# Performance work log

Measured on AMD Instinct MI355X. Metric: run time of the kernel, lower is better.

The kernel has to match this reference:

```python
import jax, jax.numpy as jnp
import numpy as np


def setup_inputs() -> dict:
    key = jax.random.key(0)
    ks = jax.random.split(key, 8)
    B, H, W, D, U = 128, 16, 48, 512, 512
    s = 1.0 / np.sqrt(D)
    return {
        "dec_hidden": jax.random.normal(ks[0], (B, D), jnp.float32),
        "enc_output": jax.random.normal(ks[1], (B, H, W, D), jnp.float32),
        "W1_w": jax.random.normal(ks[2], (D, U), jnp.float32) * s,
        "W1_b": jnp.zeros((U,), jnp.float32),
        "W2_w": jax.random.normal(ks[3], (D, U), jnp.float32) * s,
        "W2_b": jnp.zeros((U,), jnp.float32),
        "V_w": jax.random.normal(ks[4], (U, 1), jnp.float32) * (1.0 / np.sqrt(U)),
        "V_b": jnp.zeros((1,), jnp.float32),
    }


def reference(dec_hidden, enc_output, W1_w, W1_b, W2_w, W2_b, V_w, V_b):
    # dec_hidden: [B, Dd] -> [B, 1, 1, Dd]
    dec = dec_hidden[:, None, None, :]
    # W1(enc_output): [B, H, W, U]; W2(dec): [B, 1, 1, U] (broadcast add)
    h = jnp.tanh(jnp.einsum('bhwd,du->bhwu', enc_output, W1_w) + W1_b
                 + (dec @ W2_w + W2_b))
    # V(.) -> score [B, H, W, 1]
    score = jnp.einsum('bhwu,uo->bhwo', h, V_w) + V_b
    # softmax over axis=1 (H axis), matching tf.keras softmax(score, axis=1)
    attention_weights = jax.nn.softmax(score, axis=1)
    # context: sum over spatial axes -> [B, D]
    context_vector = jnp.sum(attention_weights * enc_output, axis=(1, 2))
    return context_vector, attention_weights
```

## Files before the change

kernel.cpp:

```cpp
#include <hip/hip_runtime.h>
#include <hip/hip_bf16.h>

typedef __attribute__((ext_vector_type(8))) short short8;
typedef __attribute__((ext_vector_type(4))) float f32x4;
typedef unsigned short ushort;

#define BB 128
#define HHH 16
#define WWW 48
#define DD 512
#define UU 512
#define ROWS_PER_B (HHH * WWW)
#define MTOT (BB * ROWS_PER_B)
#define BM 64
#define BN 256
#define BK 64

__device__ __forceinline__ ushort f2bf(float f) {
    return (ushort)((__float_as_uint(f) + 0x8000u) >> 16);
}

__device__ __forceinline__ void gload_lds16(const ushort* g, ushort* l) {
    __builtin_amdgcn_global_load_lds(
        (const __attribute__((address_space(1))) unsigned int*)(const void*)g,
        (__attribute__((address_space(3))) unsigned int*)(void*)l,
        16, 0, 0);
}

__global__ __launch_bounds__(256) void prep_kernel(
        const float* __restrict__ w1, const float* __restrict__ dec,
        const float* __restrict__ w2, const float* __restrict__ w1b,
        const float* __restrict__ w2b,
        ushort* __restrict__ w1p, float* __restrict__ dproj) {
    const int t = threadIdx.x;
    if (blockIdx.x < 64) {
        __shared__ __align__(16) ushort tile[64 * 72];
        const int u0 = (blockIdx.x & 7) * 64;
        const int kc = blockIdx.x >> 3;
        const int ul = t & 63;
        const int db = t >> 6;
#pragma unroll
        for (int i = 0; i < 16; ++i) {
            const int d = db + i * 4;
            tile[ul * 72 + d] = f2bf(w1[(size_t)(kc * 64 + d) * UU + u0 + ul]);
        }
        __syncthreads();
        const int u = t >> 2;
        const int s = (t & 3) * 2;
        const int x = u & 7;
        short8 v0 = *(const short8*)&tile[u * 72 + s * 8];
        short8 v1 = *(const short8*)&tile[u * 72 + s * 8 + 8];
        *(short8*)&w1p[(size_t)kc * 32768 + (u0 + u) * 64 + (( s      ^ x)) * 8] = v0;
        *(short8*)&w1p[(size_t)kc * 32768 + (u0 + u) * 64 + (((s + 1) ^ x)) * 8] = v1;
    } else {
        const int g = blockIdx.x - 64;
        const int b = g >> 1;
        const int u = (g & 1) * 256 + t;
        float acc = 0.f;
#pragma unroll 8
        for (int d = 0; d < DD; ++d)
            acc += dec[b * DD + d] * w2[(size_t)d * UU + u];
        dproj[b * UU + u] = acc + w1b[u] + w2b[u];
    }
}

__global__ __launch_bounds__(256, 4) void score_kernel(
        const float* __restrict__ enc, const ushort* __restrict__ w1p,
        const float* __restrict__ dproj, const float* __restrict__ vw,
        float* __restrict__ scorep) {
    __shared__ __align__(16) ushort Bb[BN * BK];
    __shared__ __align__(16) ushort Ab[BM * BK];

    const int tid  = threadIdx.x;
    const int lane = tid & 63;
    const int wave = tid >> 6;
    const int mbase = blockIdx.x * BM;
    const int half  = blockIdx.y;
    const int b = mbase / ROWS_PER_B;

    const int lrow = lane & 15;
    const int kgrp = lane >> 4;

    const int ar  = tid >> 2;
    const int ac  = (tid & 3) * 2;
    const float* abase = enc + (size_t)(mbase + ar) * DD + ac * 8;
    const int s0p = ( ac      ^ (ar & 7)) * 8;
    const int s1p = ((ac + 1) ^ (ar & 7)) * 8;
    const ushort* bsrc0 = w1p + half * 16384 + tid * 8;

    f32x4 acc[4][4] = {};

    for (int kc = 0; kc < 8; ++kc) {
        const ushort* bsrc = bsrc0 + (size_t)kc * 32768;
#pragma unroll
        for (int i = 0; i < 8; ++i)
            gload_lds16(bsrc + i * 2048, &Bb[tid * 8 + i * 2048]);
        {
            const float* asrc = abase + kc * 64;
            float4 a0 = ((const float4*)asrc)[0];
            float4 a1 = ((const float4*)asrc)[1];
            float4 a2 = ((const float4*)asrc)[2];
            float4 a3 = ((const float4*)asrc)[3];
            short8 w0, w1v;
            ushort* p0 = (ushort*)&w0; ushort* p1 = (ushort*)&w1v;
            p0[0]=f2bf(a0.x); p0[1]=f2bf(a0.y); p0[2]=f2bf(a0.z); p0[3]=f2bf(a0.w);
            p0[4]=f2bf(a1.x); p0[5]=f2bf(a1.y); p0[6]=f2bf(a1.z); p0[7]=f2bf(a1.w);
            p1[0]=f2bf(a2.x); p1[1]=f2bf(a2.y); p1[2]=f2bf(a2.z); p1[3]=f2bf(a2.w);
            p1[4]=f2bf(a3.x); p1[5]=f2bf(a3.y); p1[6]=f2bf(a3.z); p1[7]=f2bf(a3.w);
            *(short8*)&Ab[ar * 64 + s0p] = w0;
            *(short8*)&Ab[ar * 64 + s1p] = w1v;
        }
        __syncthreads();

#pragma unroll
        for (int kk = 0; kk < 2; ++kk) {
            const int sub = kk * 4 + kgrp;
            short8 afr[4], bfr[4];
#pragma unroll
            for (int ms = 0; ms < 4; ++ms) {
                const int r = ms * 16 + lrow;
                afr[ms] = *(const short8*)&Ab[r * 64 + (sub ^ (r & 7)) * 8];
            }
#pragma unroll
            for (int uf = 0; uf < 4; ++uf) {
                const int u = wave * 64 + uf * 16 + lrow;
                bfr[uf] = *(const short8*)&Bb[u * 64 + (sub ^ (u & 7)) * 8];
            }
#pragma unroll
            for (int ms = 0; ms < 4; ++ms)
#pragma unroll
                for (int uf = 0; uf < 4; ++uf)
                    acc[ms][uf] = __builtin_amdgcn_mfma_f32_16x16x32_bf16(
                        afr[ms], bfr[uf], acc[ms][uf], 0, 0, 0);
        }
        __syncthreads();
    }

    float part[4][4] = {};
#pragma unroll
    for (int uf = 0; uf < 4; ++uf) {
        const int u = half * 256 + wave * 64 + uf * 16 + lrow;
        const float cadd = dproj[b * UU + u];
        const float vwe  = vw[u];
#pragma unroll
        for (int ms = 0; ms < 4; ++ms)
#pragma unroll
            for (int j = 0; j < 4; ++j) {
                float x = acc[ms][uf][j] + cadd;
                x = fminf(fmaxf(x, -15.f), 15.f);
                float e = __expf(2.f * x);
                part[ms][j] += vwe * ((e - 1.f) / (e + 1.f));
            }
    }
#pragma unroll
    for (int off = 1; off < 16; off <<= 1)
#pragma unroll
        for (int ms = 0; ms < 4; ++ms)
#pragma unroll
            for (int j = 0; j < 4; ++j)
                part[ms][j] += __shfl_xor(part[ms][j], off, 64);

    float* scr = (float*)&Ab[0];
    if (lrow == 0) {
#pragma unroll
        for (int ms = 0; ms < 4; ++ms)
#pragma unroll
            for (int j = 0; j < 4; ++j)
                scr[wave * 64 + ms * 16 + kgrp * 4 + j] = part[ms][j];
    }
    __syncthreads();
    if (tid < 64)
        scorep[(size_t)half * MTOT + mbase + tid] =
            scr[tid] + scr[64 + tid] + scr[128 + tid] + scr[192 + tid];
}

__global__ __launch_bounds__(512) void ctx_kernel(
        const float* __restrict__ scorep, const float* __restrict__ enc,
        const float* __restrict__ vb,
        float* __restrict__ attn, float* __restrict__ partial) {
    __shared__ float sl[ROWS_PER_B];
    __shared__ float al[ROWS_PER_B];
    const int q = blockIdx.x;
    const int b = blockIdx.y;
    const int t = threadIdx.x;

    const float vbv = vb[0];
    for (int i = t; i < ROWS_PER_B; i += 512)
        sl[i] = scorep[b * ROWS_PER_B + i] + scorep[MTOT + b * ROWS_PER_B + i] + vbv;
    __syncthreads();

    if (t < WWW) {
        float v[HHH];
        float m = -1e30f;
#pragma unroll
        for (int h = 0; h < HHH; ++h) { v[h] = sl[h * WWW + t]; m = fmaxf(m, v[h]); }
        float sum = 0.f;
#pragma unroll
        for (int h = 0; h < HHH; ++h) { v[h] = __expf(v[h] - m); sum += v[h]; }
        const float inv = 1.f / sum;
#pragma unroll
        for (int h = 0; h < HHH; ++h) al[h * WWW + t] = v[h] * inv;
    }
    __syncthreads();

    const int rb = q * 192;
    for (int i = t; i < 192; i += 512)
        attn[b * ROWS_PER_B + rb + i] = al[rb + i];

    const int r0 = t >> 7;
    const int d4 = (t & 127) * 4;
    float4 acc = {0.f, 0.f, 0.f, 0.f};
    const float* ebase = enc + ((size_t)b * ROWS_PER_B + rb) * DD + d4;
#pragma unroll 8
    for (int i = 0; i < 48; ++i) {
        const int r = r0 + i * 4;
        const float a = al[rb + r];
        const float4 e = *(const float4*)(ebase + (size_t)r * DD);
        acc.x += a * e.x; acc.y += a * e.y; acc.z += a * e.z; acc.w += a * e.w;
    }
    *(float4*)(partial + ((size_t)((b * 4 + q) * 4 + r0)) * DD + d4) = acc;
}

__global__ void ctx_reduce_kernel(const float* __restrict__ partial,
                                  float* __restrict__ out) {
    const int qd = blockIdx.x * 256 + threadIdx.x;
    const int b = qd >> 7;
    const int d4 = (qd & 127) * 4;
    float4 s = {0.f, 0.f, 0.f, 0.f};
#pragma unroll
    for (int j = 0; j < 16; ++j) {
        const float4 p = *(const float4*)(partial + ((size_t)(b * 16 + j)) * DD + d4);
        s.x += p.x; s.y += p.y; s.z += p.z; s.w += p.w;
    }
    *(float4*)(out + (size_t)b * DD + d4) = s;
}

extern "C" void kernel_launch(void* const* d_in, const int* in_sizes, int n_in,
                              void* d_out, int out_size, void* d_ws, size_t ws_size,
                              hipStream_t stream) {
    const float* dec = (const float*)d_in[0];
    const float* enc = (const float*)d_in[1];
    const float* w1w = (const float*)d_in[2];
    const float* w1b = (const float*)d_in[3];
    const float* w2w = (const float*)d_in[4];
    const float* w2b = (const float*)d_in[5];
    const float* vw  = (const float*)d_in[6];
    const float* vb  = (const float*)d_in[7];

    float* out = (float*)d_out;
    char* ws = (char*)d_ws;
    ushort* w1p    = (ushort*)(ws);
    float* dproj   = (float*)(ws + (512 << 10));
    float* scorep  = (float*)(ws + (768 << 10));
    float* partial = (float*)(ws + (1536 << 10));

    float* ctx  = out;
    float* attn = out + BB * DD;

    prep_kernel<<<320, 256, 0, stream>>>(w1w, dec, w2w, w1b, w2b, w1p, dproj);
    score_kernel<<<dim3(MTOT / BM, 2), 256, 0, stream>>>(enc, w1p, dproj, vw, scorep);
    ctx_kernel<<<dim3(4, BB), 512, 0, stream>>>(scorep, enc, vb, attn, partial);
    ctx_reduce_kernel<<<64, 256, 0, stream>>>(partial, ctx);
}
```

Baseline: 397.6 us.

## Pre-convert encoder output to swizzled bf16 and double-buffer the score GEMM

Adds a prep pass that converts the whole fp32 encoder tensor once into a tiled, swizzled bf16 buffer in workspace. The score kernel then streams both operands straight into double-buffered LDS with async global-to-LDS loads, and the context kernel reads the bf16 copy instead of fp32. This removes the repeated fp32-to-bf16 conversion per N-half and overlaps loads with MFMA work, in exchange for an extra ~100MB write and read. It also computes the decoder projection with split-K atomics, uses an exp2/rcp tanh, and adds a blocked tile order. Context accuracy drops because enc is now bf16, and the new path only runs if the workspace is large enough.

```diff
diff --git a/kernel.cpp b/kernel.cpp
--- a/kernel.cpp
+++ b/kernel.cpp
@@ -19,7 +19,9 @@
 __device__ __forceinline__ ushort f2bf(float f) {
     return (ushort)((__float_as_uint(f) + 0x8000u) >> 16);
 }
-
+__device__ __forceinline__ float bf2f(ushort u) {
+    return __uint_as_float(((unsigned)u) << 16);
+}
 __device__ __forceinline__ void gload_lds16(const ushort* g, ushort* l) {
     __builtin_amdgcn_global_load_lds(
         (const __attribute__((address_space(1))) unsigned int*)(const void*)g,
@@ -27,7 +29,258 @@
         16, 0, 0);
 }
 
-__global__ __launch_bounds__(256) void prep_kernel(
+__global__ __launch_bounds__(256) void prep2_kernel(
+        const float* __restrict__ enc, const float* __restrict__ w1,
+        const float* __restrict__ dec, const float* __restrict__ w2,
+        ushort* __restrict__ encp, ushort* __restrict__ w1p,
+        float* __restrict__ dproj) {
+    __shared__ __align__(16) char smem[32768];
+    const int t = threadIdx.x;
+    const int bid = blockIdx.x;
+
+    if (bid < 64) {
+        const int u0 = (bid & 7) * 64;
+        const int d0 = (bid >> 3) * 64;
+        const int u  = t & 63;
+        const int bq = t >> 6;
+        float w2r[64];
+#pragma unroll
+        for (int dd = 0; dd < 64; ++dd)
+            w2r[dd] = w2[(size_t)(d0 + dd) * UU + u0 + u];
+        float* decs = (float*)smem;
+        for (int i = t; i < 8192; i += 256)
+            decs[i] = dec[(size_t)(i >> 6) * DD + d0 + (i & 63)];
+        __syncthreads();
+        for (int j = 0; j < 32; ++j) {
+            const float* dr = &decs[(bq * 32 + j) * 64];
+            float s = 0.f;
+#pragma unroll
+            for (int dd = 0; dd < 64; ++dd) s = fmaf(dr[dd], w2r[dd], s);
+            atomicAdd(&dproj[(size_t)(bq * 32 + j) * UU + u0 + u], s);
+        }
+    } else if (bid < 128) {
+        const int pb = bid - 64;
+        ushort* tile = (ushort*)smem;
+        const int u0 = (pb & 7) * 64;
+        const int kc = pb >> 3;
+        const int ul = t & 63;
+        const int db = t >> 6;
+#pragma unroll
+        for (int i = 0; i < 16; ++i) {
+            const int d = db + i * 4;
+            tile[ul * 72 + d] = f2bf(w1[(size_t)(kc * 64 + d) * UU + u0 + ul]);
+        }
+        __syncthreads();
+        const int u = t >> 2;
+        const int s = (t & 3) * 2;
+        const int x = u & 7;
+        short8 v0 = *(const short8*)&tile[u * 72 + s * 8];
+        short8 v1 = *(const short8*)&tile[u * 72 + s * 8 + 8];
+        *(short8*)&w1p[(size_t)kc * 32768 + (u0 + u) * 64 + (( s      ^ x)) * 8] = v0;
+        *(short8*)&w1p[(size_t)kc * 32768 + (u0 + u) * 64 + (((s + 1) ^ x)) * 8] = v1;
+    } else {
+        const int mt  = bid - 128;
+        const int row = t >> 2;
+        const int cb  = (t & 3) * 2;
+        const float* src = enc + ((size_t)mt * 64 + row) * DD + cb * 8;
+        ushort* dst = encp + (size_t)mt * 32768 + row * 64;
+        const int s0 = ( cb      ^ (row & 7)) * 8;
+        const int s1 = ((cb + 1) ^ (row & 7)) * 8;
+#pragma unroll
+        for (int kc = 0; kc < 8; ++kc) {
+            const float* s4 = src + kc * 64;
+            float4 a0 = ((const float4*)s4)[0];
+            float4 a1 = ((const float4*)s4)[1];
+            float4 a2 = ((const float4*)s4)[2];
+            float4 a3 = ((const float4*)s4)[3];
+            short8 w0, w1v;
+            ushort* p0 = (ushort*)&w0; ushort* p1 = (ushort*)&w1v;
+            p0[0]=f2bf(a0.x); p0[1]=f2bf(a0.y); p0[2]=f2bf(a0.z); p0[3]=f2bf(a0.w);
+            p0[4]=f2bf(a1.x); p0[5]=f2bf(a1.y); p0[6]=f2bf(a1.z); p0[7]=f2bf(a1.w);
+            p1[0]=f2bf(a2.x); p1[1]=f2bf(a2.y); p1[2]=f2bf(a2.z); p1[3]=f2bf(a2.w);
+            p1[4]=f2bf(a3.x); p1[5]=f2bf(a3.y); p1[6]=f2bf(a3.z); p1[7]=f2bf(a3.w);
+            *(short8*)&dst[kc * 4096 + s0] = w0;
+            *(short8*)&dst[kc * 4096 + s1] = w1v;
+        }
+    }
+}
+
+__global__ __launch_bounds__(256, 2) void score2_kernel(
+        const ushort* __restrict__ encp, const ushort* __restrict__ w1p,
+        const float* __restrict__ dproj, const float* __restrict__ w1b,
+        const float* __restrict__ w2b, const float* __restrict__ vw,
+        float* __restrict__ scorep) {
+    __shared__ __align__(16) ushort Bb[2][BN * BK];
+    __shared__ __align__(16) ushort Ab[2][BM * BK];
+
+    const int tid  = threadIdx.x;
+    const int lane = tid & 63;
+    const int wave = tid >> 6;
+    const int wg   = blockIdx.x;
+    const int mt   = (wg & 7) * 192 + ((wg >> 3) >> 1);
+    const int half = (wg >> 3) & 1;
+    const int mbase = mt * 64;
+    const int b = mt / 12;
+    const int lrow = lane & 15;
+    const int kgrp = lane >> 4;
+
+    const ushort* asrc0 = encp + (size_t)mt * 32768 + tid * 8;
+    const ushort* bsrc0 = w1p + half * 16384 + tid * 8;
+
+    f32x4 acc[4][4] = {};
+
+    gload_lds16(asrc0,        &Ab[0][tid * 8]);
+    gload_lds16(asrc0 + 2048, &Ab[0][tid * 8 + 2048]);
+#pragma unroll
+    for (int i = 0; i < 8; ++i)
+        gload_lds16(bsrc0 + i * 2048, &Bb[0][tid * 8 + i * 2048]);
+    asm volatile("s_waitcnt vmcnt(0)" ::: "memory");
+    __syncthreads();
+
+    for (int kc = 0; kc < 8; ++kc) {
+        const int cur = kc & 1;
+        if (kc < 7) {
+            const ushort* an = asrc0 + (kc + 1) * 4096;
+            const ushort* bn = bsrc0 + (size_t)(kc + 1) * 32768;
+            gload_lds16(an,        &Ab[cur ^ 1][tid * 8]);
+            gload_lds16(an + 2048, &Ab[cur ^ 1][tid * 8 + 2048]);
+#pragma unroll
+            for (int i = 0; i < 8; ++i)
+                gload_lds16(bn + i * 2048, &Bb[cur ^ 1][tid * 8 + i * 2048]);
+        }
+        const ushort* Bc = &Bb[cur][0];
+        const ushort* Ac = &Ab[cur][0];
+#pragma unroll
+        for (int kk = 0; kk < 2; ++kk) {
+            const int sub = kk * 4 + kgrp;
+            short8 afr[4], bfr[4];
+#pragma unroll
+            for (int ms = 0; ms < 4; ++ms) {
+                const int r = ms * 16 + lrow;
+                afr[ms] = *(const short8*)&Ac[r * 64 + (sub ^ (r & 7)) * 8];
+            }
+#pragma unroll
+            for (int uf = 0; uf < 4; ++uf) {
+                const int u = wave * 64 + uf * 16 + lrow;
+                bfr[uf] = *(const short8*)&Bc[u * 64 + (sub ^ (u & 7)) * 8];
+            }
+#pragma unroll
+            for (int ms = 0; ms < 4; ++ms)
+#pragma unroll
+                for (int uf = 0; uf < 4; ++uf)
+                    acc[ms][uf] = __builtin_amdgcn_mfma_f32_16x16x32_bf16(
+                        afr[ms], bfr[uf], acc[ms][uf], 0, 0, 0);
+        }
+        asm volatile("s_waitcnt vmcnt(0)" ::: "memory");
+        __syncthreads();
+    }
+
+    const float C2 = 2.8853900817779268f;
+    float part[4][4] = {};
+#pragma unroll
+    for (int uf = 0; uf < 4; ++uf) {
+        const int u = half * 256 + wave * 64 + uf * 16 + lrow;
+        const float cadd = dproj[b * UU + u] + w1b[u] + w2b[u];
+        const float vwe  = vw[u];
+#pragma unroll
+        for (int ms = 0; ms < 4; ++ms)
+#pragma unroll
+            for (int j = 0; j < 4; ++j) {
+                float x = acc[ms][uf][j] + cadd;
+                float e = __builtin_amdgcn_exp2f(x * C2);
+                float r = __builtin_amdgcn_rcpf(1.f + e);
+                float h = fmaf(-2.f, r, 1.f);
+                part[ms][j] = fmaf(vwe, h, part[ms][j]);
+            }
+    }
+#pragma unroll
+    for (int off = 1; off < 16; off <<= 1)
+#pragma unroll
+        for (int ms = 0; ms < 4; ++ms)
+#pragma unroll
+            for (int j = 0; j < 4; ++j)
+                part[ms][j] += __shfl_xor(part[ms][j], off, 64);
+
+    float* scr = (float*)&Ab[0][0];
+    if (lrow == 0) {
+#pragma unroll
+        for (int ms = 0; ms < 4; ++ms)
+#pragma unroll
+            for (int j = 0; j < 4; ++j)
+                scr[wave * 64 + ms * 16 + kgrp * 4 + j] = part[ms][j];
+    }
+    __syncthreads();
+    if (tid < 64)
+        scorep[(size_t)half * MTOT + mbase + tid] =
+            scr[tid] + scr[64 + tid] + scr[128 + tid] + scr[192 + tid];
+}
+
+__global__ __launch_bounds__(256) void ctx2_kernel(
+        const float* __restrict__ scorep, const ushort* __restrict__ encp,
+        const float* __restrict__ vb, float* __restrict__ attn,
+        float* __restrict__ partial) {
+    __shared__ float sl[ROWS_PER_B];
+    __shared__ float al[ROWS_PER_B];
+    const int q = blockIdx.x;
+    const int b = blockIdx.y;
+    const int t = threadIdx.x;
+    const float vbv = vb[0];
+    for (int i = t; i < ROWS_PER_B; i += 256)
+        sl[i] = scorep[b * ROWS_PER_B + i] + scorep[MTOT + b * ROWS_PER_B + i] + vbv;
+    __syncthreads();
+    if (t < WWW) {
+        float v[HHH];
+        float m = -1e30f;
+#pragma unroll
+        for (int h = 0; h < HHH; ++h) { v[h] = sl[h * WWW + t]; m = fmaxf(m, v[h]); }
+        float sum = 0.f;
+#pragma unroll
+        for (int h = 0; h < HHH; ++h) { v[h] = __expf(v[h] - m); sum += v[h]; }
+        const float inv = 1.f / sum;
+#pragma unroll
+        for (int h = 0; h < HHH; ++h) al[h * WWW + t] = v[h] * inv;
+    }
+    __syncthreads();
+    if (t < 96) attn[b * ROWS_PER_B + q * 96 + t] = al[q * 96 + t];
+
+    const int rp = t >> 6;
+    const int g8 = t & 63;
+    const int kc = g8 >> 3;
+    float fa[8] = {};
+#pragma unroll 4
+    for (int i = 0; i < 24; ++i) {
+        const int r = q * 96 + rp + i * 4;
+        const float a = al[r];
+        const size_t gr = (size_t)b * ROWS_PER_B + r;
+        const ushort* p = encp + (gr >> 6) * 32768 + kc * 4096 + (gr & 63) * 64
+                        + (((g8 & 7) ^ (r & 7)) * 8);
+        short8 v = *(const short8*)p;
+#pragma unroll
+        for (int j = 0; j < 8; ++j)
+            fa[j] = fmaf(a, bf2f((ushort)v[j]), fa[j]);
+    }
+    float* dst = partial + ((size_t)((b * 8 + q) * 4 + rp)) * DD + g8 * 8;
+    float4 o0 = {fa[0], fa[1], fa[2], fa[3]};
+    float4 o1 = {fa[4], fa[5], fa[6], fa[7]};
+    ((float4*)dst)[0] = o0;
+    ((float4*)dst)[1] = o1;
+}
+
+__global__ void reduce2_kernel(const float* __restrict__ partial,
+                               float* __restrict__ out) {
+    const int qd = blockIdx.x * 256 + threadIdx.x;
+    const int b = qd >> 7;
+    const int d4 = (qd & 127) * 4;
+    float4 s = {0.f, 0.f, 0.f, 0.f};
+#pragma unroll
+    for (int j = 0; j < 32; ++j) {
+        const float4 p = *(const float4*)(partial + ((size_t)(b * 32 + j)) * DD + d4);
+        s.x += p.x; s.y += p.y; s.z += p.z; s.w += p.w;
+    }
+    *(float4*)(out + (size_t)b * DD + d4) = s;
+}
+
+__global__ __launch_bounds__(256) void prep_fb(
         const float* __restrict__ w1, const float* __restrict__ dec,
         const float* __restrict__ w2, const float* __restrict__ w1b,
         const float* __restrict__ w2b,
@@ -64,32 +317,27 @@
     }
 }
 
-__global__ __launch_bounds__(256, 4) void score_kernel(
+__global__ __launch_bounds__(256, 4) void score_fb(
         const float* __restrict__ enc, const ushort* __restrict__ w1p,
         const float* __restrict__ dproj, const float* __restrict__ vw,
         float* __restrict__ scorep) {
     __shared__ __align__(16) ushort Bb[BN * BK];
     __shared__ __align__(16) ushort Ab[BM * BK];
-
     const int tid  = threadIdx.x;
     const int lane = tid & 63;
     const int wave = tid >> 6;
     const int mbase = blockIdx.x * BM;
     const int half  = blockIdx.y;
     const int b = mbase / ROWS_PER_B;
-
     const int lrow = lane & 15;
     const int kgrp = lane >> 4;
-
     const int ar  = tid >> 2;
     const int ac  = (tid & 3) * 2;
     const float* abase = enc + (size_t)(mbase + ar) * DD + ac * 8;
     const int s0p = ( ac      ^ (ar & 7)) * 8;
     const int s1p = ((ac + 1) ^ (ar & 7)) * 8;
     const ushort* bsrc0 = w1p + half * 16384 + tid * 8;
-
     f32x4 acc[4][4] = {};
-
     for (int kc = 0; kc < 8; ++kc) {
         const ushort* bsrc = bsrc0 + (size_t)kc * 32768;
 #pragma unroll
@@ -111,7 +359,6 @@
             *(short8*)&Ab[ar * 64 + s1p] = w1v;
         }
         __syncthreads();
-
 #pragma unroll
         for (int kk = 0; kk < 2; ++kk) {
             const int sub = kk * 4 + kgrp;
@@ -135,7 +382,6 @@
         }
         __syncthreads();
     }
-
     float part[4][4] = {};
 #pragma unroll
     for (int uf = 0; uf < 4; ++uf) {
@@ -159,7 +405,6 @@
 #pragma unroll
             for (int j = 0; j < 4; ++j)
                 part[ms][j] += __shfl_xor(part[ms][j], off, 64);
-
     float* scr = (float*)&Ab[0];
     if (lrow == 0) {
 #pragma unroll
@@ -174,7 +419,7 @@
             scr[tid] + scr[64 + tid] + scr[128 + tid] + scr[192 + tid];
 }
 
-__global__ __launch_bounds__(512) void ctx_kernel(
+__global__ __launch_bounds__(512) void ctx_fb(
         const float* __restrict__ scorep, const float* __restrict__ enc,
         const float* __restrict__ vb,
         float* __restrict__ attn, float* __restrict__ partial) {
@@ -183,12 +428,10 @@
     const int q = blockIdx.x;
     const int b = blockIdx.y;
     const int t = threadIdx.x;
-
     const float vbv = vb[0];
     for (int i = t; i < ROWS_PER_B; i += 512)
         sl[i] = scorep[b * ROWS_PER_B + i] + scorep[MTOT + b * ROWS_PER_B + i] + vbv;
     __syncthreads();
-
     if (t < WWW) {
         float v[HHH];
         float m = -1e30f;
@@ -202,11 +445,9 @@
         for (int h = 0; h < HHH; ++h) al[h * WWW + t] = v[h] * inv;
     }
     __syncthreads();
-
     const int rb = q * 192;
     for (int i = t; i < 192; i += 512)
         attn[b * ROWS_PER_B + rb + i] = al[rb + i];
-
     const int r0 = t >> 7;
     const int d4 = (t & 127) * 4;
     float4 acc = {0.f, 0.f, 0.f, 0.f};
@@ -221,8 +462,8 @@
     *(float4*)(partial + ((size_t)((b * 4 + q) * 4 + r0)) * DD + d4) = acc;
 }
 
-__global__ void ctx_reduce_kernel(const float* __restrict__ partial,
-                                  float* __restrict__ out) {
+__global__ void reduce_fb(const float* __restrict__ partial,
+                          float* __restrict__ out) {
     const int qd = blockIdx.x * 256 + threadIdx.x;
     const int b = qd >> 7;
     const int d4 = (qd & 127) * 4;
@@ -248,17 +489,37 @@
     const float* vb  = (const float*)d_in[7];
 
     float* out = (float*)d_out;
-    char* ws = (char*)d_ws;
-    ushort* w1p    = (ushort*)(ws);
-    float* dproj   = (float*)(ws + (512 << 10));
-    float* scorep  = (float*)(ws + (768 << 10));
-    float* partial = (float*)(ws + (1536 << 10));
-
     float* ctx  = out;
     float* attn = out + BB * DD;
-
-    prep_kernel<<<320, 256, 0, stream>>>(w1w, dec, w2w, w1b, w2b, w1p, dproj);
-    score_kernel<<<dim3(MTOT / BM, 2), 256, 0, stream>>>(enc, w1p, dproj, vw, scorep);
-    ctx_kernel<<<dim3(4, BB), 512, 0, stream>>>(scorep, enc, vb, attn, partial);
-    ctx_reduce_kernel<<<64, 256, 0, stream>>>(partial, ctx);
-}
+    char* ws = (char*)d_ws;
+
+    const size_t ENCP_B   = (size_t)MTOT * DD * 2;
+    const size_t W1P_B    = (size_t)UU * DD * 2;
+    const size_t DPROJ_B  = (size_t)BB * UU * 4;
+    const size_t SCOREP_B = (size_t)2 * MTOT * 4;
+    const size_t PART_B   = (size_t)BB * 32 * DD * 4;
+    const size_t NEED = ENCP_B + W1P_B + DPROJ_B + SCOREP_B + PART_B;
+
+    if (ws_size >= NEED) {
+        ushort* encp   = (ushort*)(ws);
+        ushort* w1p    = (ushort*)(ws + ENCP_B);
+        float*  dproj  = (float*)(ws + ENCP_B + W1P_B);
+        float*  scorep = (float*)(ws + ENCP_B + W1P_B + DPROJ_B);
+        float*  partial= (float*)(ws + ENCP_B + W1P_B + DPROJ_B + SCOREP_B);
+
+        hipMemsetAsync(dproj, 0, DPROJ_B, stream);
+        prep2_kernel<<<1664, 256, 0, stream>>>(enc, w1w, dec, w2w, encp, w1p, dproj);
+        score2_kernel<<<3072, 256, 0, stream>>>(encp, w1p, dproj, w1b, w2b, vw, scorep);
+        ctx2_kernel<<<dim3(8, BB), 256, 0, stream>>>(scorep, encp, vb, attn, partial);
+        reduce2_kernel<<<64, 256, 0, stream>>>(partial, ctx);
+    } else {
+        ushort* w1p    = (ushort*)(ws);
+        float*  dproj  = (float*)(ws + (512 << 10));
+        float*  scorep = (float*)(ws + (768 << 10));
+        float*  partial= (float*)(ws + (1536 << 10));
+        prep_fb<<<320, 256, 0, stream>>>(w1w, dec, w2w, w1b, w2b, w1p, dproj);
+        score_fb<<<dim3(MTOT / BM, 2), 256, 0, stream>>>(enc, w1p, dproj, vw, scorep);
+        ctx_fb<<<dim3(4, BB), 512, 0, stream>>>(scorep, enc, vb, attn, partial);
+        reduce_fb<<<64, 256, 0, stream>>>(partial, ctx);
+    }
+}
```

Measured after the change: 413.4 us. 1.04x slower.
